# Kernel optimization log

Measured on AMD Instinct MI355X. Metric: run time of the kernel, lower is better.

The kernel has to match this reference:

```python
import jax, jax.numpy as jnp
import numpy as np

HEIGHT, WIDTH = 48, 320  # output crop size (module __init__ defaults)


def setup_inputs() -> dict:
    key = jax.random.key(0)
    k1, k2 = jax.random.split(key)
    x = jax.random.normal(k1, (8, 3, 1024, 1024), dtype=jnp.float32)
    u = jax.random.uniform(k2, (8, 64, 5), dtype=jnp.float32)
    # (cx, cy, w, h, angle_deg) scaled to realistic in-image rotated boxes
    scale = jnp.array([800.0, 800.0, 250.0, 40.0, 90.0], dtype=jnp.float32)
    offset = jnp.array([100.0, 100.0, 50.0, 20.0, -45.0], dtype=jnp.float32)
    boxes = u * scale + offset
    return {"x": x, "boxes": boxes}


def _bilinear(img, sx, sy):
    # img: [C, H, W]; sx, sy: [N, Hout, Wout] source pixel coords (cv2 convention,
    # integer coords = pixel positions). Zero padding outside (BORDER_CONSTANT).
    H, W = img.shape[1], img.shape[2]
    x0 = jnp.floor(sx)
    y0 = jnp.floor(sy)
    dx = sx - x0
    dy = sy - y0
    x0i = x0.astype(jnp.int32)
    y0i = y0.astype(jnp.int32)

    def tap(xi, yi, w):
        valid = (xi >= 0) & (xi < W) & (yi >= 0) & (yi < H)
        xc = jnp.clip(xi, 0, W - 1)
        yc = jnp.clip(yi, 0, H - 1)
        return img[:, yc, xc] * (w * valid)[None]  # [C, N, Hout, Wout]

    return (tap(x0i, y0i, (1.0 - dx) * (1.0 - dy))
            + tap(x0i + 1, y0i, dx * (1.0 - dy))
            + tap(x0i, y0i + 1, (1.0 - dx) * dy)
            + tap(x0i + 1, y0i + 1, dx * dy))


def _crop_all(img, boxes):
    # img: [C, H, W]; boxes: [N, 5] = (cx, cy, bw, bh, angle_deg)
    cx, cy, bw, bh, ang = (boxes[:, i] for i in range(5))
    # cv2 rect angle is -box[4] (degrees); cv2.boxPoints corner formulas:
    theta = -ang * (jnp.pi / 180.0)
    b = jnp.cos(theta) * 0.5
    a = jnp.sin(theta) * 0.5
    p0x = cx - a * bh - b * bw; p0y = cy + b * bh - a * bw  # -> dst (0, H)
    p1x = cx + a * bh - b * bw; p1y = cy - b * bh - a * bw  # -> dst (0, 0)
    p2x = 2.0 * cx - p0x;       p2y = 2.0 * cy - p0y        # -> dst (W, 0)
    # Rect -> rect perspective transform degenerates to this exact affine map.
    u = (jnp.arange(WIDTH, dtype=jnp.float32) / WIDTH)[None, None, :]    # [1,1,Wout]
    v = (jnp.arange(HEIGHT, dtype=jnp.float32) / HEIGHT)[None, :, None]  # [1,Hout,1]
    sx = p1x[:, None, None] + u * (p2x - p1x)[:, None, None] + v * (p0x - p1x)[:, None, None]
    sy = p1y[:, None, None] + u * (p2y - p1y)[:, None, None] + v * (p0y - p1y)[:, None, None]
    crops = _bilinear(img, sx, sy)           # [C, N, Hout, Wout]
    return jnp.transpose(crops, (1, 0, 2, 3))  # [N, C, Hout, Wout]


def reference(x, boxes):
    # x: [B, C, H, W]; boxes: [B, N, 5] -> patches [B*N, C, HEIGHT, WIDTH]
    patches = jax.vmap(_crop_all)(x, boxes)  # [B, N, C, Hout, Wout]
    B, N = patches.shape[0], patches.shape[1]
    return patches.reshape(B * N, patches.shape[2], HEIGHT, WIDTH)
```

## Files before the change

### kernel.cpp

```cpp
#include <hip/hip_runtime.h>
#include <math.h>

#define HOUT 48
#define WOUT 320
#define NB   8
#define NBOX 64
#define NC   3
#define IMH  1024
#define IMW  1024

#define PIX_PER_CROP (HOUT * WOUT)
#define BLK 256
#define BLKS_PER_CROP (PIX_PER_CROP / BLK)

__global__ __launch_bounds__(BLK) void rot_crop_kernel(
    const float* __restrict__ x,
    const float* __restrict__ boxes,
    float* __restrict__ out)
{
    const int bn  = blockIdx.x / BLKS_PER_CROP;
    const int pix = (blockIdx.x % BLKS_PER_CROP) * BLK + threadIdx.x;
    const int j = pix % WOUT;
    const int i = pix / WOUT;
    const int b = bn / NBOX;

    const float* box = boxes + bn * 5;
    const float cx  = box[0];
    const float cy  = box[1];
    const float bw  = box[2];
    const float bh  = box[3];
    const float ang = box[4];

    const float theta = ang * (-3.14159265358979323846f / 180.0f);
    float st, ct;
    __sincosf(theta, &st, &ct);
    const float bb = ct * 0.5f;
    const float aa = st * 0.5f;

    const float p0x = cx - aa * bh - bb * bw;
    const float p0y = cy + bb * bh - aa * bw;
    const float p1x = cx + aa * bh - bb * bw;
    const float p1y = cy - bb * bh - aa * bw;
    const float p2x = 2.0f * cx - p0x;
    const float p2y = 2.0f * cy - p0y;

    const float u = (float)j * (1.0f / (float)WOUT);
    const float v = (float)i * (1.0f / (float)HOUT);

    const float sx = p1x + u * (p2x - p1x) + v * (p0x - p1x);
    const float sy = p1y + u * (p2y - p1y) + v * (p0y - p1y);

    const float x0f = floorf(sx);
    const float y0f = floorf(sy);
    const float dx = sx - x0f;
    const float dy = sy - y0f;
    const int x0i = (int)x0f;
    const int y0i = (int)y0f;
    const int x1i = x0i + 1;
    const int y1i = y0i + 1;

    const bool vx0 = (x0i >= 0) & (x0i < IMW);
    const bool vx1 = (x1i >= 0) & (x1i < IMW);
    const bool vy0 = (y0i >= 0) & (y0i < IMH);
    const bool vy1 = (y1i >= 0) & (y1i < IMH);

    const int xc0 = min(max(x0i, 0), IMW - 1);
    const int xc1 = min(max(x1i, 0), IMW - 1);
    const int yc0 = min(max(y0i, 0), IMH - 1);
    const int yc1 = min(max(y1i, 0), IMH - 1);

    const float w00 = (1.0f - dx) * (1.0f - dy) * (float)(vx0 && vy0);
    const float w10 = dx * (1.0f - dy)          * (float)(vx1 && vy0);
    const float w01 = (1.0f - dx) * dy          * (float)(vx0 && vy1);
    const float w11 = dx * dy                   * (float)(vx1 && vy1);

    const long long o00 = (long long)yc0 * IMW + xc0;
    const long long o10 = (long long)yc0 * IMW + xc1;
    const long long o01 = (long long)yc1 * IMW + xc0;
    const long long o11 = (long long)yc1 * IMW + xc1;

    const float* img = x + (long long)b * NC * IMH * IMW;
    float* op = out + (long long)bn * NC * PIX_PER_CROP + pix;

#pragma unroll
    for (int c = 0; c < NC; ++c) {
        const float* ch = img + (long long)c * (IMH * IMW);
        const float acc = ch[o00] * w00 + ch[o10] * w10
                        + ch[o01] * w01 + ch[o11] * w11;
        op[(long long)c * PIX_PER_CROP] = acc;
    }
}

extern "C" void kernel_launch(void* const* d_in, const int* in_sizes, int n_in,
                              void* d_out, int out_size, void* d_ws, size_t ws_size,
                              hipStream_t stream) {
    const float* x     = (const float*)d_in[0];
    const float* boxes = (const float*)d_in[1];
    float* out         = (float*)d_out;

    const int nblocks = NB * NBOX * BLKS_PER_CROP;
    rot_crop_kernel<<<nblocks, BLK, 0, stream>>>(x, boxes, out);
}
```

Measured before the change: 225.9 us.

## Use 16x16 output tiles with 16x4 wavefront patches and XCD-aware block swizzle

Each block now covers a 16x16 square output tile instead of 256 consecutive pixels, and each wavefront covers a 16x4 patch. Because rotated source footprints are compact, this is meant to improve cache-line reuse of the gathered input pixels. Block indices are remapped so that consecutive hardware block IDs, which are distributed round-robin over the 8 XCDs, land on contiguous tiles of the same crop, improving L2 locality per XCD. Offsets switch to 32-bit ints to reduce address arithmetic. Output writes become 16-wide row segments, so stores are less contiguous.

```diff
diff --git a/kernel.cpp b/kernel.cpp
--- a/kernel.cpp
+++ b/kernel.cpp
@@ -11,17 +11,27 @@
 
 #define PIX_PER_CROP (HOUT * WOUT)
 #define BLK 256
-#define BLKS_PER_CROP (PIX_PER_CROP / BLK)
+#define TILES_Y (HOUT / 16)
+#define TILES_X (WOUT / 16)
+#define BLKS_PER_CROP (TILES_Y * TILES_X)
+#define NBLOCKS (NB * NBOX * BLKS_PER_CROP)
 
 __global__ __launch_bounds__(BLK) void rot_crop_kernel(
     const float* __restrict__ x,
     const float* __restrict__ boxes,
     float* __restrict__ out)
 {
-    const int bn  = blockIdx.x / BLKS_PER_CROP;
-    const int pix = (blockIdx.x % BLKS_PER_CROP) * BLK + threadIdx.x;
-    const int j = pix % WOUT;
-    const int i = pix / WOUT;
+    const int bid = (blockIdx.x & 7) * (NBLOCKS / 8) + (blockIdx.x >> 3);
+
+    const int bn = bid / BLKS_PER_CROP;
+    const int t  = bid % BLKS_PER_CROP;
+    const int bi = t / TILES_X;
+    const int bj = t % TILES_X;
+
+    const int lane = threadIdx.x & 63;
+    const int wv   = threadIdx.x >> 6;
+    const int i = bi * 16 + wv * 4 + (lane >> 4);
+    const int j = bj * 16 + (lane & 15);
     const int b = bn / NBOX;
 
     const float* box = boxes + bn * 5;
@@ -74,20 +84,20 @@
     const float w01 = (1.0f - dx) * dy          * (float)(vx0 && vy1);
     const float w11 = dx * dy                   * (float)(vx1 && vy1);
 
-    const long long o00 = (long long)yc0 * IMW + xc0;
-    const long long o10 = (long long)yc0 * IMW + xc1;
-    const long long o01 = (long long)yc1 * IMW + xc0;
-    const long long o11 = (long long)yc1 * IMW + xc1;
+    const int o00 = yc0 * IMW + xc0;
+    const int o10 = yc0 * IMW + xc1;
+    const int o01 = yc1 * IMW + xc0;
+    const int o11 = yc1 * IMW + xc1;
 
     const float* img = x + (long long)b * NC * IMH * IMW;
-    float* op = out + (long long)bn * NC * PIX_PER_CROP + pix;
+    float* op = out + (long long)bn * NC * PIX_PER_CROP + i * WOUT + j;
 
 #pragma unroll
     for (int c = 0; c < NC; ++c) {
-        const float* ch = img + (long long)c * (IMH * IMW);
+        const float* ch = img + c * (IMH * IMW);
         const float acc = ch[o00] * w00 + ch[o10] * w10
                         + ch[o01] * w01 + ch[o11] * w11;
-        op[(long long)c * PIX_PER_CROP] = acc;
+        op[c * PIX_PER_CROP] = acc;
     }
 }
 
@@ -98,6 +108,5 @@
     const float* boxes = (const float*)d_in[1];
     float* out         = (float*)d_out;
 
-    const int nblocks = NB * NBOX * BLKS_PER_CROP;
-    rot_crop_kernel<<<nblocks, BLK, 0, stream>>>(x, boxes, out);
+    rot_crop_kernel<<<NBLOCKS, BLK, 0, stream>>>(x, boxes, out);
 }
```

After: 223.1 us. About the same (-1.2%).
